# Optimization experiments

Measured on AMD Instinct MI355X. Metric: run time of the kernel, lower is better.

## Reference

```python
import jax, jax.numpy as jnp
import numpy as np

N_NODES = 50000
N_EDGES = 1600000
IN_DIM, HID_DIM, OUT_DIM = 512, 256, 128
N_IDX = 8192


def _graph_conv(x, src, dst, W, b, n_nodes):
    # DGL GraphConv, norm='both': D_dst^{-1/2} A D_src^{-1/2} x W + b
    ones = jnp.ones(src.shape[0], dtype=x.dtype)
    deg_out = jax.ops.segment_sum(ones, src, num_segments=n_nodes)
    deg_in = jax.ops.segment_sum(ones, dst, num_segments=n_nodes)
    ns = jax.lax.rsqrt(jnp.maximum(deg_out, 1.0))  # source norm
    nd = jax.lax.rsqrt(jnp.maximum(deg_in, 1.0))   # dest norm
    msg = (x * ns[:, None])[src]                   # gather [E, F]
    agg = jax.ops.segment_sum(msg, dst, num_segments=n_nodes)
    return (agg * nd[:, None]) @ W + b


def _gcn(x, src, dst, W1, b1, W2, b2, n_nodes):
    h = jax.nn.relu(_graph_conv(x, src, dst, W1, b1, n_nodes))
    return _graph_conv(h, src, dst, W2, b2, n_nodes)


def setup_inputs() -> dict:
    key = jax.random.key(0)
    ks = jax.random.split(key, 16)
    d = {
        'raw1': jax.random.normal(ks[0], (N_NODES, IN_DIM), jnp.float32),
        'raw2': jax.random.normal(ks[1], (N_NODES, IN_DIM), jnp.float32),
        'src1': jax.random.randint(ks[2], (N_EDGES,), 0, N_NODES),
        'dst1': jax.random.randint(ks[3], (N_EDGES,), 0, N_NODES),
        'src2': jax.random.randint(ks[4], (N_EDGES,), 0, N_NODES),
        'dst2': jax.random.randint(ks[5], (N_EDGES,), 0, N_NODES),
        'index': jax.random.randint(ks[6], (N_IDX,), 0, N_NODES),
    }
    def lin(k, fi, fo):
        s = 1.0 / np.sqrt(fi)
        return jax.random.uniform(k, (fi, fo), jnp.float32, -s, s)
    d['e1_W1'] = lin(ks[7], IN_DIM, HID_DIM); d['e1_b1'] = jnp.zeros(HID_DIM, jnp.float32)
    d['e1_W2'] = lin(ks[8], HID_DIM, OUT_DIM); d['e1_b2'] = jnp.zeros(OUT_DIM, jnp.float32)
    d['e2_W1'] = lin(ks[9], IN_DIM, HID_DIM); d['e2_b1'] = jnp.zeros(HID_DIM, jnp.float32)
    d['e2_W2'] = lin(ks[10], HID_DIM, OUT_DIM); d['e2_b2'] = jnp.zeros(OUT_DIM, jnp.float32)
    return d


def reference(raw1, raw2, src1, dst1, src2, dst2, index,
              e1_W1, e1_b1, e1_W2, e1_b2, e2_W1, e2_b1, e2_W2, e2_b2):
    n = raw1.shape[0]
    c1 = _gcn(raw1, src1, dst1, e1_W1, e1_b1, e1_W2, e1_b2, n)[index]
    c2 = _gcn(raw2, src2, dst2, e2_W1, e2_b1, e2_W2, e2_b2, n)[index]
    # F.normalize(dim=1), eps=1e-12
    c1 = c1 / jnp.maximum(jnp.linalg.norm(c1, axis=1, keepdims=True), 1e-12)
    c2 = c2 / jnp.maximum(jnp.linalg.norm(c2, axis=1, keepdims=True), 1e-12)
    z1 = c1 @ c1.T
    z2 = c2 @ c2.T
    z3 = c1 @ c2.T
    z3 = (z3 + z3.T) * 0.5
    z = (z1 + z2 + z3) * (1.0 / 3.0)
    return jnp.triu(z)
```

## Files before the change

kernel.cpp:

```cpp
#include <hip/hip_runtime.h>
#include <hip/hip_bf16.h>

using u16 = unsigned short;
using u32 = unsigned int;

typedef __attribute__((ext_vector_type(8))) short short8;
typedef __attribute__((ext_vector_type(4))) float f32x4;

__device__ __forceinline__ u16 f2bf_u16(float f) {
    __hip_bfloat16 h = __float2bfloat16(f);
    return __builtin_bit_cast(u16, h);
}
__device__ __forceinline__ float bfu(u32 u) { return __uint_as_float(u << 16); }

static constexpr int NN = 50000;
static constexpr int NE = 1600000;
static constexpr int NIDX = 8192;
static constexpr int NRANGE = 8;
static constexpr int RN = NN / NRANGE;
static constexpr int HCH = 16;
static constexpr int NK = NN * NRANGE;
static constexpr int SAB = (NK + 4095) / 4096;
static constexpr int CAPB = 262144;
static constexpr int PEB = 8192;
static constexpr int PGX = (NE + PEB - 1) / PEB;
static constexpr int CVB = 640;
static constexpr int PSTG = 1536;
static constexpr int ZLB = 64 * 63 / 2;
static constexpr int ZHB = ZLB / 2;
static constexpr int ZUB = 64 * 65 / 2;
static constexpr int AGB = NN / 4;
static constexpr int MT = (NN + 127) / 128;
static constexpr int SCX = 256;


__global__ __launch_bounds__(256)
void partition_kernel(const int* __restrict__ s1, const int* __restrict__ d1,
                      const int* __restrict__ s2, const int* __restrict__ d2,
                      int* __restrict__ bcur, u32* __restrict__ ebuf_d, u16* __restrict__ ebuf_s,
                      const float* __restrict__ W1a, const float* __restrict__ W1b,
                      const float* __restrict__ W2a, const float* __restrict__ W2b,
                      u16* __restrict__ W1t, u16* __restrict__ W2t) {
    if (blockIdx.x >= PGX) {
        int o = (blockIdx.x - PGX) + CVB * blockIdx.y;
        int idx = o * 256 + threadIdx.x;
        if (idx < 131072) {
            int k = idx >> 8, n = idx & 255;
            W1t[(size_t)n * 512 + k] = f2bf_u16(W1a[idx]);
        } else if (idx < 262144) {
            int j = idx - 131072;
            int k = j >> 8, n = j & 255;
            W1t[(size_t)131072 + (size_t)n * 512 + k] = f2bf_u16(W1b[j]);
        } else if (idx < 294912) {
            int j = idx - 262144;
            int k = j >> 7, n = j & 127;
            W2t[(size_t)n * 256 + k] = f2bf_u16(W2a[j]);
        } else if (idx < 327680) {
            int j = idx - 294912;
            int k = j >> 7, n = j & 127;
            W2t[(size_t)32768 + (size_t)n * 256 + k] = f2bf_u16(W2b[j]);
        }
        return;
    }
    __shared__ u32 stage_d[8][PSTG];
    __shared__ u16 stage_s[8][PSTG];
    __shared__ int cnt_d[8], cnt_s[8], base_d[8], base_s[8];
    int enc = blockIdx.y;
    const int* s = enc ? s2 : s1;
    const int* d = enc ? d2 : d1;
    if (threadIdx.x < 8) { cnt_d[threadIdx.x] = 0; cnt_s[threadIdx.x] = 0; }
    __syncthreads();
    int* bc_d = bcur + enc * 16;
    int* bc_s = bcur + enc * 16 + 8;
    u32* bd = ebuf_d + (size_t)enc * 8 * CAPB;
    u16* bs = ebuf_s + (size_t)enc * 8 * CAPB;
    int e0 = blockIdx.x * PEB;
    int e1 = min(e0 + PEB, NE);
    for (int e = e0 + threadIdx.x * 4; e < e1; e += 1024) {
        int4 sv = *(const int4*)(s + e);
        int4 dv = *(const int4*)(d + e);
        #pragma unroll
        for (int j = 0; j < 4; ++j) {
            int src = j == 0 ? sv.x : j == 1 ? sv.y : j == 2 ? sv.z : sv.w;
            int dst = j == 0 ? dv.x : j == 1 ? dv.y : j == 2 ? dv.z : dv.w;
            int rd = dst / RN;
            u32 entry = (u32)src | ((u32)(dst - rd * RN) << 16);
            int slot = atomicAdd(&cnt_d[rd], 1);
            if (slot < PSTG) stage_d[rd][slot] = entry;
            else { int gp = atomicAdd(&bc_d[rd], 1); bd[(size_t)rd * CAPB + gp] = entry; }
            int rs = src / RN;
            int slot2 = atomicAdd(&cnt_s[rs], 1);
            if (slot2 < PSTG) stage_s[rs][slot2] = (u16)(src - rs * RN);
            else { int gp = atomicAdd(&bc_s[rs], 1); bs[(size_t)rs * CAPB + gp] = (u16)(src - rs * RN); }
        }
    }
    __syncthreads();
    if (threadIdx.x < 8) {
        int b = threadIdx.x;
        base_d[b] = atomicAdd(&bc_d[b], min(cnt_d[b], PSTG));
        base_s[b] = atomicAdd(&bc_s[b], min(cnt_s[b], PSTG));
    }
    __syncthreads();
    #pragma unroll
    for (int b = 0; b < 8; ++b) {
        int nb = min(cnt_d[b], PSTG);
        for (int i = threadIdx.x; i < nb; i += 256)
            bd[(size_t)b * CAPB + base_d[b] + i] = stage_d[b][i];
        int ns = min(cnt_s[b], PSTG);
        for (int i = threadIdx.x; i < ns; i += 256)
            bs[(size_t)b * CAPB + base_s[b] + i] = stage_s[b][i];
    }
}


__global__ __launch_bounds__(256)
void bhist_kernel(const u32* __restrict__ ebuf_d, const u16* __restrict__ ebuf_s,
                  const int* __restrict__ bcur,
                  u32* __restrict__ partial2, u32* __restrict__ partial_out) {
    __shared__ u32 sh[RN * 2];
    int stripe = blockIdx.x & 7, chunk = blockIdx.x >> 3;
    int enc = blockIdx.y & 1, type = blockIdx.y >> 1;
    if (type == 0) {
        for (int i = threadIdx.x; i < RN * 2; i += 256) sh[i] = 0;
        __syncthreads();
        int size = bcur[enc * 16 + stripe];
        int cs = (size + HCH - 1) / HCH;
        int lo = chunk * cs, hi = min(lo + cs, size);
        const u32* b = ebuf_d + ((size_t)enc * 8 + stripe) * CAPB;
        for (int i = lo + threadIdx.x; i < hi; i += 256) {
            u32 e = b[i];
            u32 idx = (e >> 16) * 8 + (e & 0xffffu) / RN;
            atomicAdd(&sh[idx >> 2], 1u << ((idx & 3) * 8));
        }
        __syncthreads();
        u32* p2 = partial2 + ((size_t)enc * HCH + chunk) * (NN * 2) + stripe * (RN * 2);
        for (int i = threadIdx.x; i < RN * 2; i += 256) p2[i] = sh[i];
    } else {
        for (int i = threadIdx.x; i < RN / 2; i += 256) sh[i] = 0;
        __syncthreads();
        int size = bcur[enc * 16 + 8 + stripe];
        int cs = (size + HCH - 1) / HCH;
        int lo = chunk * cs, hi = min(lo + cs, size);
        const u16* b = ebuf_s + ((size_t)enc * 8 + stripe) * CAPB;
        for (int i = lo + threadIdx.x; i < hi; i += 256) {
            u32 sl = b[i];
            atomicAdd(&sh[sl >> 1], 1u << ((sl & 1) * 16));
        }
        __syncthreads();
        u32* po = partial_out + ((size_t)enc * HCH + chunk) * (NN / 2) + stripe * (RN / 2);
        for (int i = threadIdx.x; i < RN / 2; i += 256) po[i] = sh[i];
    }
}

__global__ void reduce_hist_kernel(const u32* __restrict__ partial2,
                                   const u32* __restrict__ partial_out,
                                   int* __restrict__ deg2, float* __restrict__ norms) {
    int i = blockIdx.x * blockDim.x + threadIdx.x;
    if (i >= 2 * NN) return;
    int enc = i / NN;
    int dst = i - enc * NN;
    int cnt[8];
    #pragma unroll
    for (int r = 0; r < 8; ++r) cnt[r] = 0;
    for (int c = 0; c < HCH; ++c) {
        const u32* p = partial2 + ((size_t)enc * HCH + c) * (NN * 2) + dst * 2;
        u32 w0 = p[0], w1 = p[1];
        cnt[0] += w0 & 0xff; cnt[1] += (w0 >> 8) & 0xff; cnt[2] += (w0 >> 16) & 0xff; cnt[3] += w0 >> 24;
        cnt[4] += w1 & 0xff; cnt[5] += (w1 >> 8) & 0xff; cnt[6] += (w1 >> 16) & 0xff; cnt[7] += w1 >> 24;
    }
    int* dp = deg2 + (size_t)enc * NK + dst * 8;
    int din = 0;
    #pragma unroll
    for (int r = 0; r < 8; ++r) { dp[r] = cnt[r]; din += cnt[r]; }
    norms[(enc * 2 + 1) * NN + dst] = rsqrtf(fmaxf((float)din, 1.f));
    int dout = 0;
    for (int c = 0; c < HCH; ++c) {
        u32 w = partial_out[((size_t)enc * HCH + c) * (NN / 2) + (dst >> 1)];
        dout += (w >> ((dst & 1) * 16)) & 0xffff;
    }
    norms[(enc * 2 + 0) * NN + dst] = rsqrtf(fmaxf((float)dout, 1.f));
}


__global__ __launch_bounds__(1024)
void scanA_kernel(const int* __restrict__ deg2, int* __restrict__ rp2_all, int* __restrict__ tot) {
    int enc = blockIdx.y;
    const int* deg = deg2 + (size_t)enc * NK;
    int* rp = rp2_all + (size_t)enc * (NK + 1);
    __shared__ int wsum[16];
    int t = threadIdx.x, lane = t & 63, wid = t >> 6;
    int i0 = blockIdx.x * 4096 + t * 4;
    int4 v = make_int4(0, 0, 0, 0);
    bool in = (i0 + 3 < NK);
    if (in) v = *(const int4*)(deg + i0);
    int s = v.x + v.y + v.z + v.w;
    int x = s;
    #pragma unroll
    for (int d = 1; d < 64; d <<= 1) {
        int y = __shfl_up(x, d, 64);
        if (lane >= d) x += y;
    }
    if (lane == 63) wsum[wid] = x;
    __syncthreads();
    if (t == 0) {
        int run = 0;
        #pragma unroll
        for (int w = 0; w < 16; ++w) { int q = wsum[w]; wsum[w] = run; run += q; }
        tot[enc * SAB + blockIdx.x] = run;
    }
    __syncthreads();
    if (in) {
        int excl = wsum[wid] + x - s;
        rp[i0] = excl;
        rp[i0 + 1] = excl + v.x;
        rp[i0 + 2] = excl + v.x + v.y;
        rp[i0 + 3] = excl + v.x + v.y + v.z;
    }
}

__global__ __launch_bounds__(256)
void scanC_kernel(int* __restrict__ rp2_all, int* __restrict__ cur2_all, const int* __restrict__ tot) {
    int enc = blockIdx.y;
    int* rp = rp2_all + (size_t)enc * (NK + 1);
    int* cur = cur2_all + (size_t)enc * NK;
    int nA = blockIdx.x >> 2;
    int part = 0;
    for (int i = threadIdx.x; i < nA; i += 256) part += tot[enc * SAB + i];
    #pragma unroll
    for (int d = 1; d < 64; d <<= 1) part += __shfl_xor(part, d, 64);
    __shared__ int red[4];
    __shared__ int soff;
    int lane = threadIdx.x & 63, wv = threadIdx.x >> 6;
    if (lane == 0) red[wv] = part;
    __syncthreads();
    if (threadIdx.x == 0) soff = red[0] + red[1] + red[2] + red[3];
    __syncthreads();
    int off = soff;
    int idx = (blockIdx.x * 256 + threadIdx.x) * 4;
    if (idx < NK) {
        int4 v = *(const int4*)(rp + idx);
        v.x += off; v.y += off; v.z += off; v.w += off;
        *(int4*)(rp + idx) = v;
        *(int4*)(cur + idx) = v;
    }
    if (blockIdx.x == 0 && threadIdx.x == 0) rp[NK] = NE;
}


__device__ __forceinline__ void scatter_body(const u32* __restrict__ ebuf_d,
                                             const int* __restrict__ bcur,
                                             int* __restrict__ cur2_all, u16* __restrict__ csr_all,
                                             int stripe, int chunk, int enc) {
    int size = bcur[enc * 16 + stripe];
    int cs = (size + 63) / 64;
    int lo = chunk * cs, hi = min(lo + cs, size);
    const u32* b = ebuf_d + ((size_t)enc * 8 + stripe) * CAPB;
    int* cursor = cur2_all + (size_t)enc * NK;
    u16* csr = csr_all + (size_t)enc * NE;
    int base = stripe * RN;
    for (int i = lo + threadIdx.x; i < hi; i += 256) {
        u32 e = b[i];
        int src = e & 0xffff;
        int dst = base + (int)(e >> 16);
        int key = dst * 8 + src / RN;
        int pos = atomicAdd(&cursor[key], 1);
        csr[pos] = (u16)src;
    }
}


template<bool A_F32, bool OUT_BF16, bool TRIANG, bool SCALE>
__device__ __forceinline__ void gemm_device(const void* __restrict__ A_, const u16* __restrict__ Bt,
                                            void* __restrict__ C_, const float* __restrict__ rowscale,
                                            int M, int N, int K, int it, int jt, u16* smem) {
    int t = threadIdx.x;
    int brow = it * 128, bcol = jt * 128;
    float* Cf = (float*)C_;
    u16* As = smem;
    u16* Bs = smem + 128 * 40;
    int lane = t & 63, wv = t >> 6;
    int wr = wv >> 1, wc = wv & 1;
    f32x4 acc[4][4];
    #pragma unroll
    for (int m = 0; m < 4; ++m)
        #pragma unroll
        for (int n = 0; n < 4; ++n) acc[m][n] = f32x4{0.f, 0.f, 0.f, 0.f};

    float4 a_f0[4], a_f1[4];
    uint4  a_h0[2], a_h1[2];
    uint4  b_h0[2], b_h1[2];

#define LOADT(S, kk) do {                                                          \
    if constexpr (A_F32) {                                                         \
        const float* A = (const float*)A_;                                         \
        _Pragma("unroll")                                                          \
        for (int p = 0; p < 4; ++p) {                                              \
            int r = p * 32 + (t >> 3), c = (t & 7) * 4;                            \
            int gr = brow + r;                                                     \
            a_f##S[p] = make_float4(0.f, 0.f, 0.f, 0.f);                           \
            if (gr < M) a_f##S[p] = *(const float4*)(A + (size_t)gr * K + (kk) + c); \
        }                                                                          \
    } else {                                                                       \
        const u16* A = (const u16*)A_;                                             \
        _Pragma("unroll")                                                          \
        for (int p = 0; p < 2; ++p) {                                              \
            int r = p * 64 + (t >> 2), c = (t & 3) * 8;                            \
            int gr = brow + r;                                                     \
            a_h##S[p] = make_uint4(0u, 0u, 0u, 0u);                                \
            if (gr < M) a_h##S[p] = *(const uint4*)(A + (size_t)gr * K + (kk) + c); \
        }                                                                          \
    }                                                                              \
    _Pragma("unroll")                                                              \
    for (int p = 0; p < 2; ++p) {                                                  \
        int r = p * 64 + (t >> 2), c = (t & 3) * 8;                                \
        int gn = bcol + r;                                                         \
        b_h##S[p] = make_uint4(0u, 0u, 0u, 0u);                                    \
        if (gn < N) b_h##S[p] = *(const uint4*)(Bt + (size_t)gn * K + (kk) + c);   \
    }                                                                              \
} while (0)

#define STORET(S) do {                                                             \
    if constexpr (A_F32) {                                                         \
        _Pragma("unroll")                                                          \
        for (int p = 0; p < 4; ++p) {                                              \
            int r = p * 32 + (t >> 3), c = (t & 7) * 4;                            \
            u32 lo = (u32)f2bf_u16(a_f##S[p].x) | ((u32)f2bf_u16(a_f##S[p].y) << 16); \
            u32 hi = (u32)f2bf_u16(a_f##S[p].z) | ((u32)f2bf_u16(a_f##S[p].w) << 16); \
            *(uint2*)&As[r * 40 + c] = make_uint2(lo, hi);                         \
        }                                                                          \
    } else {                                                                       \
        _Pragma("unroll")                                                          \
        for (int p = 0; p < 2; ++p) {                                              \
            int r = p * 64 + (t >> 2), c = (t & 3) * 8;                            \
            *(uint4*)&As[r * 40 + c] = a_h##S[p];                                  \
        }                                                                          \
    }                                                                              \
    _Pragma("unroll")                                                              \
    for (int p = 0; p < 2; ++p) {                                                  \
        int r = p * 64 + (t >> 2), c = (t & 3) * 8;                                \
        *(uint4*)&Bs[r * 40 + c] = b_h##S[p];                                      \
    }                                                                              \
} while (0)

    auto compute = [&]() {
        int kg = (lane >> 4) * 8;
        short8 av[4], bv[4];
        #pragma unroll
        for (int m = 0; m < 4; ++m)
            av[m] = *(const short8*)&As[(wr * 64 + m * 16 + (lane & 15)) * 40 + kg];
        #pragma unroll
        for (int n = 0; n < 4; ++n)
            bv[n] = *(const short8*)&Bs[(wc * 64 + n * 16 + (lane & 15)) * 40 + kg];
        #pragma unroll
        for (int m = 0; m < 4; ++m)
            #pragma unroll
            for (int n = 0; n < 4; ++n)
                acc[m][n] = __builtin_amdgcn_mfma_f32_16x16x32_bf16(av[m], bv[n], acc[m][n], 0, 0, 0);
    };

    LOADT(0, 0);
    LOADT(1, 32);
    for (int k0 = 0; k0 < K; k0 += 64) {
        STORET(0);
        __syncthreads();
        if (k0 + 64 < K) LOADT(0, k0 + 64);
        compute();
        __syncthreads();
        STORET(1);
        __syncthreads();
        if (k0 + 96 < K) LOADT(1, k0 + 96);
        compute();
        __syncthreads();
    }
#undef LOADT
#undef STORET

    const int lane15 = lane & 15, lanehi = lane >> 4;
    if (OUT_BF16) {
        u16* stg = smem + wv * 1024;
        #pragma unroll
        for (int m = 0; m < 4; ++m) {
            #pragma unroll
            for (int n = 0; n < 4; ++n)
                #pragma unroll
                for (int r = 0; r < 4; ++r) {
                    float v = acc[m][n][r];
                    if (SCALE) v *= rowscale[brow + wr * 64 + m * 16 + lanehi * 4 + r];
                    stg[(lanehi * 4 + r) * 64 + n * 16 + lane15] = f2bf_u16(v);
                }
            #pragma unroll
            for (int pass = 0; pass < 2; ++pass) {
                int lr = pass * 8 + (lane >> 3);
                int grow = brow + wr * 64 + m * 16 + lr;
                uint4 w = *(uint4*)&stg[lr * 64 + (lane & 7) * 8];
                if (grow < M)
                    *(uint4*)((u16*)C_ + (size_t)grow * N + bcol + wc * 64 + (lane & 7) * 8) = w;
            }
        }
    } else {
        float* stg = (float*)smem + wv * 1024;
        #pragma unroll
        for (int m = 0; m < 4; ++m) {
            #pragma unroll
            for (int n = 0; n < 4; ++n)
                #pragma unroll
                for (int r = 0; r < 4; ++r) {
                    int row = brow + wr * 64 + m * 16 + lanehi * 4 + r;
                    int col = bcol + wc * 64 + n * 16 + lane15;
                    float v = acc[m][n][r];
                    if (SCALE) v *= rowscale[row];
                    if (TRIANG && col < row) v = 0.f;
                    stg[(lanehi * 4 + r) * 64 + n * 16 + lane15] = v;
                }
            #pragma unroll
            for (int pass = 0; pass < 4; ++pass) {
                int lr = pass * 4 + lanehi;
                int grow = brow + wr * 64 + m * 16 + lr;
                f32x4 w = *(f32x4*)&stg[lr * 64 + lane15 * 4];
                if (grow < M) {
                    float* dp = Cf + (size_t)grow * N + bcol + wc * 64 + lane15 * 4;
                    if (TRIANG) __builtin_nontemporal_store(w, (f32x4*)dp);
                    else *(f32x4*)dp = w;
                }
            }
        }
    }
}

__global__ __launch_bounds__(256)
void gemm1scat_kernel(const float* __restrict__ raw0, const float* __restrict__ raw1,
                      const u16* __restrict__ W1t, u16* __restrict__ Y1,
                      const float* __restrict__ norms,
                      const u32* __restrict__ ebuf_d, const int* __restrict__ bcur,
                      int* __restrict__ tick, int* __restrict__ cur2, u16* __restrict__ csr_all) {
    if (blockIdx.x >= MT) {
        u32 lin = blockIdx.x + gridDim.x * (blockIdx.y + gridDim.y * blockIdx.z);
        int stripe = lin & 7;
        __shared__ int tsh;
        if (threadIdx.x == 0) tsh = atomicAdd(&tick[stripe], 1);
        __syncthreads();
        int tkt = tsh;
        scatter_body(ebuf_d, bcur, cur2, csr_all, stripe, tkt & 63, tkt >> 6);
        return;
    }
    __shared__ alignas(16) u16 smem[128 * 40 * 2];
    int enc = blockIdx.z;
    gemm_device<true, true, false, true>(
        enc ? raw1 : raw0, W1t + (size_t)enc * 512 * 256,
        Y1 + (size_t)enc * NN * 256, norms + (size_t)2 * enc * NN,
        NN, 256, 512, blockIdx.x, blockIdx.y, smem);
}

__global__ __launch_bounds__(256)
void gemm2_kernel(const u16* __restrict__ H1, const u16* __restrict__ W2t,
                  u16* __restrict__ Y2, const float* __restrict__ norms) {
    __shared__ alignas(16) u16 smem[128 * 40 * 2];
    int enc = blockIdx.z;
    gemm_device<false, true, false, true>(
        H1 + (size_t)enc * NN * 256, W2t + (size_t)enc * 256 * 128,
        Y2 + (size_t)enc * NN * 128, norms + (size_t)2 * enc * NN,
        NN, 128, 256, blockIdx.x, 0, smem);
}

__global__ __launch_bounds__(256)
void zgemm_kernel(const u16* __restrict__ R, float* __restrict__ out) {
    int b = blockIdx.x;
    int i = (int)((129.0f - sqrtf(129.f * 129.f - 8.f * b)) * 0.5f);
    while ((i + 1) * (129 - (i + 1)) / 2 <= b) ++i;
    while (i * (129 - i) / 2 > b) --i;
    int it = i;
    int jt = i + (b - i * (129 - i) / 2);
    __shared__ alignas(16) u16 smem[128 * 40 * 2];
    gemm_device<false, false, true, false>(R, R, out, nullptr, NIDX, NIDX, 256, it, jt, smem);
}


template<int F, bool RELU, bool OUT_BF16, bool ZFILL>
__global__ __launch_bounds__(256)
void agg_kernel(const u16* __restrict__ Yall, const int* __restrict__ rp2_all,
                const u16* __restrict__ csr_all, const float* __restrict__ norms,
                const float* __restrict__ bias0, const float* __restrict__ bias1,
                void* __restrict__ out_all, float* __restrict__ zout) {
    constexpr int VPL = F / 64;
    int enc = blockIdx.y;
    int bid = blockIdx.x;
    if (ZFILL) {
        if (bid < ZHB) {
            int b = enc * ZHB + bid;
            float fit = (sqrtf(8.f * b + 1.f) + 1.f) * 0.5f;
            int it = (int)fit;
            if (it * (it - 1) / 2 > b) --it;
            else if ((it + 1) * it / 2 <= b) ++it;
            int jt = b - it * (it - 1) / 2;
            int brow = it * 128, bcol = jt * 128;
            f32x4 z = {0.f, 0.f, 0.f, 0.f};
            #pragma unroll
            for (int pq = 0; pq < 16; ++pq) {
                int idx = pq * 256 + threadIdx.x;
                int r = idx >> 5, c4 = idx & 31;
                __builtin_nontemporal_store(z, (f32x4*)(zout + (size_t)(brow + r) * NIDX + bcol + c4 * 4));
            }
            return;
        }
        bid -= ZHB;
    }
    const u16* Y = Yall + (size_t)enc * NN * F;
    const int* rp2 = rp2_all + (size_t)enc * (NK + 1);
    const u16* csr = csr_all + (size_t)enc * NE;
    const float* nd = norms + (size_t)(2 * enc + 1) * NN;
    const float* bias = enc ? bias1 : bias0;
    int lane = threadIdx.x & 63;
    int node = bid * 4 + (threadIdx.x >> 6);
    int e0 = rp2[node * 8], e1 = rp2[node * 8 + 8];
    float acc[VPL];
    #pragma unroll
    for (int j = 0; j < VPL; ++j) acc[j] = 0.f;
    const int off = lane * VPL;

    int e = e0;
    for (; e < e1 && (e & 7) != 0; ++e) {
        int s = csr[e];
        uint2 d = *(const uint2*)(Y + (size_t)s * F + off);
        acc[0] += bfu(d.x & 0xffffu); acc[1] += bfu(d.x >> 16);
        acc[2] += bfu(d.y & 0xffffu); acc[3] += bfu(d.y >> 16);
    }
    for (; e + 16 <= e1; e += 16) {
        uint4 ia = *(const uint4*)(csr + e);
        uint4 ib = *(const uint4*)(csr + e + 8);
        int s0 = ia.x & 0xffff, s1 = ia.x >> 16, s2 = ia.y & 0xffff, s3 = ia.y >> 16;
        int s4 = ia.z & 0xffff, s5 = ia.z >> 16, s6 = ia.w & 0xffff, s7 = ia.w >> 16;
        int s8 = ib.x & 0xffff, s9 = ib.x >> 16, sa = ib.y & 0xffff, sb = ib.y >> 16;
        int sc = ib.z & 0xffff, sd = ib.z >> 16, se = ib.w & 0xffff, sf = ib.w >> 16;
        uint2 d0 = *(const uint2*)(Y + (size_t)s0 * F + off);
        uint2 d1 = *(const uint2*)(Y + (size_t)s1 * F + off);
        uint2 d2 = *(const uint2*)(Y + (size_t)s2 * F + off);
        uint2 d3 = *(const uint2*)(Y + (size_t)s3 * F + off);
        uint2 d4 = *(const uint2*)(Y + (size_t)s4 * F + off);
        uint2 d5 = *(const uint2*)(Y + (size_t)s5 * F + off);
        uint2 d6 = *(const uint2*)(Y + (size_t)s6 * F + off);
        uint2 d7 = *(const uint2*)(Y + (size_t)s7 * F + off);
        uint2 d8 = *(const uint2*)(Y + (size_t)s8 * F + off);
        uint2 d9 = *(const uint2*)(Y + (size_t)s9 * F + off);
        uint2 da = *(const uint2*)(Y + (size_t)sa * F + off);
        uint2 db = *(const uint2*)(Y + (size_t)sb * F + off);
        uint2 dc = *(const uint2*)(Y + (size_t)sc * F + off);
        uint2 dd = *(const uint2*)(Y + (size_t)sd * F + off);
        uint2 de = *(const uint2*)(Y + (size_t)se * F + off);
        uint2 df = *(const uint2*)(Y + (size_t)sf * F + off);
        acc[0] += bfu(d0.x & 0xffffu); acc[1] += bfu(d0.x >> 16); acc[2] += bfu(d0.y & 0xffffu); acc[3] += bfu(d0.y >> 16);
        acc[0] += bfu(d1.x & 0xffffu); acc[1] += bfu(d1.x >> 16); acc[2] += bfu(d1.y & 0xffffu); acc[3] += bfu(d1.y >> 16);
        acc[0] += bfu(d2.x & 0xffffu); acc[1] += bfu(d2.x >> 16); acc[2] += bfu(d2.y & 0xffffu); acc[3] += bfu(d2.y >> 16);
        acc[0] += bfu(d3.x & 0xffffu); acc[1] += bfu(d3.x >> 16); acc[2] += bfu(d3.y & 0xffffu); acc[3] += bfu(d3.y >> 16);
        acc[0] += bfu(d4.x & 0xffffu); acc[1] += bfu(d4.x >> 16); acc[2] += bfu(d4.y & 0xffffu); acc[3] += bfu(d4.y >> 16);
        acc[0] += bfu(d5.x & 0xffffu); acc[1] += bfu(d5.x >> 16); acc[2] += bfu(d5.y & 0xffffu); acc[3] += bfu(d5.y >> 16);
        acc[0] += bfu(d6.x & 0xffffu); acc[1] += bfu(d6.x >> 16); acc[2] += bfu(d6.y & 0xffffu); acc[3] += bfu(d6.y >> 16);
        acc[0] += bfu(d7.x & 0xffffu); acc[1] += bfu(d7.x >> 16); acc[2] += bfu(d7.y & 0xffffu); acc[3] += bfu(d7.y >> 16);
        acc[0] += bfu(d8.x & 0xffffu); acc[1] += bfu(d8.x >> 16); acc[2] += bfu(d8.y & 0xffffu); acc[3] += bfu(d8.y >> 16);
        acc[0] += bfu(d9.x & 0xffffu); acc[1] += bfu(d9.x >> 16); acc[2] += bfu(d9.y & 0xffffu); acc[3] += bfu(d9.y >> 16);
        acc[0] += bfu(da.x & 0xffffu); acc[1] += bfu(da.x >> 16); acc[2] += bfu(da.y & 0xffffu); acc[3] += bfu(da.y >> 16);
        acc[0] += bfu(db.x & 0xffffu); acc[1] += bfu(db.x >> 16); acc[2] += bfu(db.y & 0xffffu); acc[3] += bfu(db.y >> 16);
        acc[0] += bfu(dc.x & 0xffffu); acc[1] += bfu(dc.x >> 16); acc[2] += bfu(dc.y & 0xffffu); acc[3] += bfu(dc.y >> 16);
        acc[0] += bfu(dd.x & 0xffffu); acc[1] += bfu(dd.x >> 16); acc[2] += bfu(dd.y & 0xffffu); acc[3] += bfu(dd.y >> 16);
        acc[0] += bfu(de.x & 0xffffu); acc[1] += bfu(de.x >> 16); acc[2] += bfu(de.y & 0xffffu); acc[3] += bfu(de.y >> 16);
        acc[0] += bfu(df.x & 0xffffu); acc[1] += bfu(df.x >> 16); acc[2] += bfu(df.y & 0xffffu); acc[3] += bfu(df.y >> 16);
    }
    for (; e + 8 <= e1; e += 8) {
        uint4 iv = *(const uint4*)(csr + e);
        int s0 = iv.x & 0xffff, s1 = iv.x >> 16;
        int s2 = iv.y & 0xffff, s3 = iv.y >> 16;
        int s4 = iv.z & 0xffff, s5 = iv.z >> 16;
        int s6 = iv.w & 0xffff, s7 = iv.w >> 16;
        uint2 d0 = *(const uint2*)(Y + (size_t)s0 * F + off);
        uint2 d1 = *(const uint2*)(Y + (size_t)s1 * F + off);
        uint2 d2 = *(const uint2*)(Y + (size_t)s2 * F + off);
        uint2 d3 = *(const uint2*)(Y + (size_t)s3 * F + off);
        uint2 d4 = *(const uint2*)(Y + (size_t)s4 * F + off);
        uint2 d5 = *(const uint2*)(Y + (size_t)s5 * F + off);
        uint2 d6 = *(const uint2*)(Y + (size_t)s6 * F + off);
        uint2 d7 = *(const uint2*)(Y + (size_t)s7 * F + off);
        acc[0] += bfu(d0.x & 0xffffu); acc[1] += bfu(d0.x >> 16); acc[2] += bfu(d0.y & 0xffffu); acc[3] += bfu(d0.y >> 16);
        acc[0] += bfu(d1.x & 0xffffu); acc[1] += bfu(d1.x >> 16); acc[2] += bfu(d1.y & 0xffffu); acc[3] += bfu(d1.y >> 16);
        acc[0] += bfu(d2.x & 0xffffu); acc[1] += bfu(d2.x >> 16); acc[2] += bfu(d2.y & 0xffffu); acc[3] += bfu(d2.y >> 16);
        acc[0] += bfu(d3.x & 0xffffu); acc[1] += bfu(d3.x >> 16); acc[2] += bfu(d3.y & 0xffffu); acc[3] += bfu(d3.y >> 16);
        acc[0] += bfu(d4.x & 0xffffu); acc[1] += bfu(d4.x >> 16); acc[2] += bfu(d4.y & 0xffffu); acc[3] += bfu(d4.y >> 16);
        acc[0] += bfu(d5.x & 0xffffu); acc[1] += bfu(d5.x >> 16); acc[2] += bfu(d5.y & 0xffffu); acc[3] += bfu(d5.y >> 16);
        acc[0] += bfu(d6.x & 0xffffu); acc[1] += bfu(d6.x >> 16); acc[2] += bfu(d6.y & 0xffffu); acc[3] += bfu(d6.y >> 16);
        acc[0] += bfu(d7.x & 0xffffu); acc[1] += bfu(d7.x >> 16); acc[2] += bfu(d7.y & 0xffffu); acc[3] += bfu(d7.y >> 16);
    }
    for (; e < e1; ++e) {
        int s = csr[e];
        uint2 d = *(const uint2*)(Y + (size_t)s * F + off);
        acc[0] += bfu(d.x & 0xffffu); acc[1] += bfu(d.x >> 16);
        acc[2] += bfu(d.y & 0xffffu); acc[3] += bfu(d.y >> 16);
    }

    float ndv = nd[node];
    #pragma unroll
    for (int j = 0; j < VPL; ++j) {
        float o = acc[j] * ndv + bias[off + j];
        if (RELU) o = fmaxf(o, 0.f);
        ((u16*)out_all)[(size_t)enc * NN * F + (size_t)node * F + off + j] = f2bf_u16(o);
    }
}


__global__ __launch_bounds__(256)
void aggr_kernel(const u16* __restrict__ Y2all, const int* __restrict__ rp2_all,
                 const u16* __restrict__ csr_all, const float* __restrict__ norms,
                 const float* __restrict__ b2a, const float* __restrict__ b2b,
                 const int* __restrict__ index, u16* __restrict__ R) {
    int pos = blockIdx.x * 4 + (threadIdx.x >> 6);
    int lane = threadIdx.x & 63;
    int node = index[pos];
    const int off = lane * 2;
    float cx[2], cy[2];
    #pragma unroll
    for (int enc = 0; enc < 2; ++enc) {
        const u16* Y = Y2all + (size_t)enc * NN * 128;
        const int* rp2 = rp2_all + (size_t)enc * (NK + 1);
        const u16* csr = csr_all + (size_t)enc * NE;
        int e0 = rp2[node * 8], e1 = rp2[node * 8 + 8];
        float a0 = 0.f, a1 = 0.f;
        int e = e0;
        for (; e < e1 && (e & 7) != 0; ++e) {
            int s = csr[e];
            u32 d = *(const u32*)(Y + (size_t)s * 128 + off);
            a0 += bfu(d & 0xffffu); a1 += bfu(d >> 16);
        }
        for (; e + 8 <= e1; e += 8) {
            uint4 iv = *(const uint4*)(csr + e);
            int s0 = iv.x & 0xffff, s1 = iv.x >> 16;
            int s2 = iv.y & 0xffff, s3 = iv.y >> 16;
            int s4 = iv.z & 0xffff, s5 = iv.z >> 16;
            int s6 = iv.w & 0xffff, s7 = iv.w >> 16;
            u32 d0 = *(const u32*)(Y + (size_t)s0 * 128 + off);
            u32 d1 = *(const u32*)(Y + (size_t)s1 * 128 + off);
            u32 d2 = *(const u32*)(Y + (size_t)s2 * 128 + off);
            u32 d3 = *(const u32*)(Y + (size_t)s3 * 128 + off);
            u32 d4 = *(const u32*)(Y + (size_t)s4 * 128 + off);
            u32 d5 = *(const u32*)(Y + (size_t)s5 * 128 + off);
            u32 d6 = *(const u32*)(Y + (size_t)s6 * 128 + off);
            u32 d7 = *(const u32*)(Y + (size_t)s7 * 128 + off);
            a0 += bfu(d0 & 0xffffu); a1 += bfu(d0 >> 16);
            a0 += bfu(d1 & 0xffffu); a1 += bfu(d1 >> 16);
            a0 += bfu(d2 & 0xffffu); a1 += bfu(d2 >> 16);
            a0 += bfu(d3 & 0xffffu); a1 += bfu(d3 >> 16);
            a0 += bfu(d4 & 0xffffu); a1 += bfu(d4 >> 16);
            a0 += bfu(d5 & 0xffffu); a1 += bfu(d5 >> 16);
            a0 += bfu(d6 & 0xffffu); a1 += bfu(d6 >> 16);
            a0 += bfu(d7 & 0xffffu); a1 += bfu(d7 >> 16);
        }
        for (; e < e1; ++e) {
            int s = csr[e];
            u32 d = *(const u32*)(Y + (size_t)s * 128 + off);
            a0 += bfu(d & 0xffffu); a1 += bfu(d >> 16);
        }
        float ndv = norms[(2 * enc + 1) * NN + node];
        const float* bias = enc ? b2b : b2a;
        float o0 = a0 * ndv + bias[off];
        float o1 = a1 * ndv + bias[off + 1];
        float ss = o0 * o0 + o1 * o1;
        #pragma unroll
        for (int dshf = 1; dshf < 64; dshf <<= 1) ss += __shfl_xor(ss, dshf, 64);
        float inv = 1.f / fmaxf(sqrtf(ss), 1e-12f);
        cx[enc] = o0 * inv;
        cy[enc] = o1 * inv;
    }
    const float c2 = 0.5f, c3 = 0.28867513459481287f;
    u16* Rp = R + (size_t)pos * 256;
    u32 w0 = (u32)f2bf_u16((cx[0] + cx[1]) * c2) | ((u32)f2bf_u16((cy[0] + cy[1]) * c2) << 16);
    u32 w1 = (u32)f2bf_u16((cx[0] - cx[1]) * c3) | ((u32)f2bf_u16((cy[0] - cy[1]) * c3) << 16);
    *(u32*)(Rp + off) = w0;
    *(u32*)(Rp + 128 + off) = w1;
}


extern "C" void kernel_launch(void* const* d_in, const int* in_sizes, int n_in,
                              void* d_out, int out_size, void* d_ws, size_t ws_size,
                              hipStream_t stream) {
    (void)in_sizes; (void)n_in; (void)out_size; (void)ws_size;
    const float* raw0 = (const float*)d_in[0];
    const float* raw1 = (const float*)d_in[1];
    const int* src1 = (const int*)d_in[2], *dst1 = (const int*)d_in[3];
    const int* src2 = (const int*)d_in[4], *dst2 = (const int*)d_in[5];
    const int* index = (const int*)d_in[6];
    const float* W1a = (const float*)d_in[7];  const float* b1a = (const float*)d_in[8];
    const float* W2a = (const float*)d_in[9];  const float* b2a = (const float*)d_in[10];
    const float* W1b = (const float*)d_in[11]; const float* b1b = (const float*)d_in[12];
    const float* W2b = (const float*)d_in[13]; const float* b2b = (const float*)d_in[14];

    char* wp = (char*)d_ws;
    auto alloc = [&](size_t bytes) -> char* {
        char* r = wp;
        wp += (bytes + 255) & ~(size_t)255;
        return r;
    };
    float* norms   = (float*)alloc((size_t)4 * NN * 4);
    int*   deg2    = (int*)alloc((size_t)2 * NK * 4);
    int*   rp2     = (int*)alloc((size_t)2 * (NK + 1) * 4);
    int*   cur2    = (int*)alloc((size_t)2 * NK * 4);
    int*   tot     = (int*)alloc((size_t)2 * SAB * 4);
    int*   bcur    = (int*)alloc(48 * 4);
    u16*   csr_all = (u16*)alloc((size_t)2 * NE * 2);
    u16*   W1t     = (u16*)alloc((size_t)2 * 512 * 256 * 2);
    u16*   W2t     = (u16*)alloc((size_t)2 * 256 * 128 * 2);
    u16*   Y1      = (u16*)alloc((size_t)2 * NN * 256 * 2);
    u16*   H1      = (u16*)alloc((size_t)2 * NN * 256 * 2);
    u16*   Y2      = (u16*)alloc((size_t)2 * NN * 128 * 2);
    float* H2      = (float*)alloc((size_t)2 * NN * 128 * 4);
    u16*   R       = (u16*)alloc((size_t)NIDX * 256 * 2);
    int*   tick    = bcur + 32;
    u32* partial2    = (u32*)Y1;
    u32* partial_out = (u32*)H1;
    u32* ebuf_d      = (u32*)Y2;
    u16* ebuf_s      = (u16*)H2;

    hipMemsetAsync(bcur, 0, 48 * 4, stream);
    partition_kernel<<<dim3(PGX + CVB, 2), 256, 0, stream>>>(
        src1, dst1, src2, dst2, bcur, ebuf_d, ebuf_s, W1a, W1b, W2a, W2b, W1t, W2t);
    bhist_kernel<<<dim3(8 * HCH, 4), 256, 0, stream>>>(ebuf_d, ebuf_s, bcur, partial2, partial_out);
    reduce_hist_kernel<<<(2 * NN + 255) / 256, 256, 0, stream>>>(partial2, partial_out, deg2, norms);
    scanA_kernel<<<dim3(SAB, 2), 1024, 0, stream>>>(deg2, rp2, tot);
    scanC_kernel<<<dim3((NK / 4 + 255) / 256, 2), 256, 0, stream>>>(rp2, cur2, tot);

    gemm1scat_kernel<<<dim3(MT + SCX, 2, 2), 256, 0, stream>>>(
        raw0, raw1, W1t, Y1, norms, ebuf_d, bcur, tick, cur2, csr_all);
    agg_kernel<256, true, true, true><<<dim3(ZHB + AGB, 2), 256, 0, stream>>>(
        Y1, rp2, csr_all, norms, b1a, b1b, H1, (float*)d_out);
    gemm2_kernel<<<dim3(MT, 1, 2), 256, 0, stream>>>(H1, W2t, Y2, norms);
    aggr_kernel<<<NIDX / 4, 256, 0, stream>>>(Y2, rp2, csr_all, norms, b2a, b2b, index, R);
    zgemm_kernel<<<dim3(ZUB, 1, 1), 256, 0, stream>>>(R, (float*)d_out);
}
```

Baseline: 528.6 us.

## Restructure layer-1 aggregation to process eight nodes per wave range by range

Replaces the templated one-node-per-wave aggregation with a dedicated layer-1 kernel. Each wave now owns eight destination nodes and walks the eight source-node ranges in an outer loop, so the gathers for all eight nodes hit the same slice of Y1 together. The aim is better L2 reuse of the gathered feature rows, and the output is written as packed vector stores. In exchange it drops the 16- and 8-edge unrolled gather loops, leaving a scalar per-edge loop with less memory-level parallelism, and it launches far fewer blocks.

```diff
diff --git a/kernel.cpp b/kernel.cpp
--- a/kernel.cpp
+++ b/kernel.cpp
@@ -29,7 +29,7 @@
 static constexpr int ZLB = 64 * 63 / 2;
 static constexpr int ZHB = ZLB / 2;
 static constexpr int ZUB = 64 * 65 / 2;
-static constexpr int AGB = NN / 4;
+static constexpr int NAGB = (NN + 31) / 32;
 static constexpr int MT = (NN + 127) / 128;
 static constexpr int SCX = 256;
 
@@ -475,132 +475,79 @@
 }
 
 
-template<int F, bool RELU, bool OUT_BF16, bool ZFILL>
-__global__ __launch_bounds__(256)
-void agg_kernel(const u16* __restrict__ Yall, const int* __restrict__ rp2_all,
-                const u16* __restrict__ csr_all, const float* __restrict__ norms,
-                const float* __restrict__ bias0, const float* __restrict__ bias1,
-                void* __restrict__ out_all, float* __restrict__ zout) {
-    constexpr int VPL = F / 64;
+__global__ __launch_bounds__(256)
+void agg1_kernel(const u16* __restrict__ Yall, const int* __restrict__ rp2_all,
+                 const u16* __restrict__ csr_all, const float* __restrict__ norms,
+                 const float* __restrict__ bias0, const float* __restrict__ bias1,
+                 u16* __restrict__ out_all, float* __restrict__ zout) {
     int enc = blockIdx.y;
     int bid = blockIdx.x;
-    if (ZFILL) {
-        if (bid < ZHB) {
-            int b = enc * ZHB + bid;
-            float fit = (sqrtf(8.f * b + 1.f) + 1.f) * 0.5f;
-            int it = (int)fit;
-            if (it * (it - 1) / 2 > b) --it;
-            else if ((it + 1) * it / 2 <= b) ++it;
-            int jt = b - it * (it - 1) / 2;
-            int brow = it * 128, bcol = jt * 128;
-            f32x4 z = {0.f, 0.f, 0.f, 0.f};
-            #pragma unroll
-            for (int pq = 0; pq < 16; ++pq) {
-                int idx = pq * 256 + threadIdx.x;
-                int r = idx >> 5, c4 = idx & 31;
-                __builtin_nontemporal_store(z, (f32x4*)(zout + (size_t)(brow + r) * NIDX + bcol + c4 * 4));
-            }
-            return;
-        }
-        bid -= ZHB;
-    }
-    const u16* Y = Yall + (size_t)enc * NN * F;
+    if (bid < ZHB) {
+        int b = enc * ZHB + bid;
+        float fit = (sqrtf(8.f * b + 1.f) + 1.f) * 0.5f;
+        int it = (int)fit;
+        if (it * (it - 1) / 2 > b) --it;
+        else if ((it + 1) * it / 2 <= b) ++it;
+        int jt = b - it * (it - 1) / 2;
+        int brow = it * 128, bcol = jt * 128;
+        f32x4 z = {0.f, 0.f, 0.f, 0.f};
+        #pragma unroll
+        for (int pq = 0; pq < 16; ++pq) {
+            int idx = pq * 256 + threadIdx.x;
+            int r = idx >> 5, c4 = idx & 31;
+            __builtin_nontemporal_store(z, (f32x4*)(zout + (size_t)(brow + r) * NIDX + bcol + c4 * 4));
+        }
+        return;
+    }
+    bid -= ZHB;
+    const u16* Y = Yall + (size_t)enc * NN * 256;
     const int* rp2 = rp2_all + (size_t)enc * (NK + 1);
     const u16* csr = csr_all + (size_t)enc * NE;
     const float* nd = norms + (size_t)(2 * enc + 1) * NN;
     const float* bias = enc ? bias1 : bias0;
-    int lane = threadIdx.x & 63;
-    int node = bid * 4 + (threadIdx.x >> 6);
-    int e0 = rp2[node * 8], e1 = rp2[node * 8 + 8];
-    float acc[VPL];
-    #pragma unroll
-    for (int j = 0; j < VPL; ++j) acc[j] = 0.f;
-    const int off = lane * VPL;
-
-    int e = e0;
-    for (; e < e1 && (e & 7) != 0; ++e) {
-        int s = csr[e];
-        uint2 d = *(const uint2*)(Y + (size_t)s * F + off);
-        acc[0] += bfu(d.x & 0xffffu); acc[1] += bfu(d.x >> 16);
-        acc[2] += bfu(d.y & 0xffffu); acc[3] += bfu(d.y >> 16);
-    }
-    for (; e + 16 <= e1; e += 16) {
-        uint4 ia = *(const uint4*)(csr + e);
-        uint4 ib = *(const uint4*)(csr + e + 8);
-        int s0 = ia.x & 0xffff, s1 = ia.x >> 16, s2 = ia.y & 0xffff, s3 = ia.y >> 16;
-        int s4 = ia.z & 0xffff, s5 = ia.z >> 16, s6 = ia.w & 0xffff, s7 = ia.w >> 16;
-        int s8 = ib.x & 0xffff, s9 = ib.x >> 16, sa = ib.y & 0xffff, sb = ib.y >> 16;
-        int sc = ib.z & 0xffff, sd = ib.z >> 16, se = ib.w & 0xffff, sf = ib.w >> 16;
-        uint2 d0 = *(const uint2*)(Y + (size_t)s0 * F + off);
-        uint2 d1 = *(const uint2*)(Y + (size_t)s1 * F + off);
-        uint2 d2 = *(const uint2*)(Y + (size_t)s2 * F + off);
-        uint2 d3 = *(const uint2*)(Y + (size_t)s3 * F + off);
-        uint2 d4 = *(const uint2*)(Y + (size_t)s4 * F + off);
-        uint2 d5 = *(const uint2*)(Y + (size_t)s5 * F + off);
-        uint2 d6 = *(const uint2*)(Y + (size_t)s6 * F + off);
-        uint2 d7 = *(const uint2*)(Y + (size_t)s7 * F + off);
-        uint2 d8 = *(const uint2*)(Y + (size_t)s8 * F + off);
-        uint2 d9 = *(const uint2*)(Y + (size_t)s9 * F + off);
-        uint2 da = *(const uint2*)(Y + (size_t)sa * F + off);
-        uint2 db = *(const uint2*)(Y + (size_t)sb * F + off);
-        uint2 dc = *(const uint2*)(Y + (size_t)sc * F + off);
-        uint2 dd = *(const uint2*)(Y + (size_t)sd * F + off);
-        uint2 de = *(const uint2*)(Y + (size_t)se * F + off);
-        uint2 df = *(const uint2*)(Y + (size_t)sf * F + off);
-        acc[0] += bfu(d0.x & 0xffffu); acc[1] += bfu(d0.x >> 16); acc[2] += bfu(d0.y & 0xffffu); acc[3] += bfu(d0.y >> 16);
-        acc[0] += bfu(d1.x & 0xffffu); acc[1] += bfu(d1.x >> 16); acc[2] += bfu(d1.y & 0xffffu); acc[3] += bfu(d1.y >> 16);
-        acc[0] += bfu(d2.x & 0xffffu); acc[1] += bfu(d2.x >> 16); acc[2] += bfu(d2.y & 0xffffu); acc[3] += bfu(d2.y >> 16);
-        acc[0] += bfu(d3.x & 0xffffu); acc[1] += bfu(d3.x >> 16); acc[2] += bfu(d3.y & 0xffffu); acc[3] += bfu(d3.y >> 16);
-        acc[0] += bfu(d4.x & 0xffffu); acc[1] += bfu(d4.x >> 16); acc[2] += bfu(d4.y & 0xffffu); acc[3] += bfu(d4.y >> 16);
-        acc[0] += bfu(d5.x & 0xffffu); acc[1] += bfu(d5.x >> 16); acc[2] += bfu(d5.y & 0xffffu); acc[3] += bfu(d5.y >> 16);
-        acc[0] += bfu(d6.x & 0xffffu); acc[1] += bfu(d6.x >> 16); acc[2] += bfu(d6.y & 0xffffu); acc[3] += bfu(d6.y >> 16);
-        acc[0] += bfu(d7.x & 0xffffu); acc[1] += bfu(d7.x >> 16); acc[2] += bfu(d7.y & 0xffffu); acc[3] += bfu(d7.y >> 16);
-        acc[0] += bfu(d8.x & 0xffffu); acc[1] += bfu(d8.x >> 16); acc[2] += bfu(d8.y & 0xffffu); acc[3] += bfu(d8.y >> 16);
-        acc[0] += bfu(d9.x & 0xffffu); acc[1] += bfu(d9.x >> 16); acc[2] += bfu(d9.y & 0xffffu); acc[3] += bfu(d9.y >> 16);
-        acc[0] += bfu(da.x & 0xffffu); acc[1] += bfu(da.x >> 16); acc[2] += bfu(da.y & 0xffffu); acc[3] += bfu(da.y >> 16);
-        acc[0] += bfu(db.x & 0xffffu); acc[1] += bfu(db.x >> 16); acc[2] += bfu(db.y & 0xffffu); acc[3] += bfu(db.y >> 16);
-        acc[0] += bfu(dc.x & 0xffffu); acc[1] += bfu(dc.x >> 16); acc[2] += bfu(dc.y & 0xffffu); acc[3] += bfu(dc.y >> 16);
-        acc[0] += bfu(dd.x & 0xffffu); acc[1] += bfu(dd.x >> 16); acc[2] += bfu(dd.y & 0xffffu); acc[3] += bfu(dd.y >> 16);
-        acc[0] += bfu(de.x & 0xffffu); acc[1] += bfu(de.x >> 16); acc[2] += bfu(de.y & 0xffffu); acc[3] += bfu(de.y >> 16);
-        acc[0] += bfu(df.x & 0xffffu); acc[1] += bfu(df.x >> 16); acc[2] += bfu(df.y & 0xffffu); acc[3] += bfu(df.y >> 16);
-    }
-    for (; e + 8 <= e1; e += 8) {
-        uint4 iv = *(const uint4*)(csr + e);
-        int s0 = iv.x & 0xffff, s1 = iv.x >> 16;
-        int s2 = iv.y & 0xffff, s3 = iv.y >> 16;
-        int s4 = iv.z & 0xffff, s5 = iv.z >> 16;
-        int s6 = iv.w & 0xffff, s7 = iv.w >> 16;
-        uint2 d0 = *(const uint2*)(Y + (size_t)s0 * F + off);
-        uint2 d1 = *(const uint2*)(Y + (size_t)s1 * F + off);
-        uint2 d2 = *(const uint2*)(Y + (size_t)s2 * F + off);
-        uint2 d3 = *(const uint2*)(Y + (size_t)s3 * F + off);
-        uint2 d4 = *(const uint2*)(Y + (size_t)s4 * F + off);
-        uint2 d5 = *(const uint2*)(Y + (size_t)s5 * F + off);
-        uint2 d6 = *(const uint2*)(Y + (size_t)s6 * F + off);
-        uint2 d7 = *(const uint2*)(Y + (size_t)s7 * F + off);
-        acc[0] += bfu(d0.x & 0xffffu); acc[1] += bfu(d0.x >> 16); acc[2] += bfu(d0.y & 0xffffu); acc[3] += bfu(d0.y >> 16);
-        acc[0] += bfu(d1.x & 0xffffu); acc[1] += bfu(d1.x >> 16); acc[2] += bfu(d1.y & 0xffffu); acc[3] += bfu(d1.y >> 16);
-        acc[0] += bfu(d2.x & 0xffffu); acc[1] += bfu(d2.x >> 16); acc[2] += bfu(d2.y & 0xffffu); acc[3] += bfu(d2.y >> 16);
-        acc[0] += bfu(d3.x & 0xffffu); acc[1] += bfu(d3.x >> 16); acc[2] += bfu(d3.y & 0xffffu); acc[3] += bfu(d3.y >> 16);
-        acc[0] += bfu(d4.x & 0xffffu); acc[1] += bfu(d4.x >> 16); acc[2] += bfu(d4.y & 0xffffu); acc[3] += bfu(d4.y >> 16);
-        acc[0] += bfu(d5.x & 0xffffu); acc[1] += bfu(d5.x >> 16); acc[2] += bfu(d5.y & 0xffffu); acc[3] += bfu(d5.y >> 16);
-        acc[0] += bfu(d6.x & 0xffffu); acc[1] += bfu(d6.x >> 16); acc[2] += bfu(d6.y & 0xffffu); acc[3] += bfu(d6.y >> 16);
-        acc[0] += bfu(d7.x & 0xffffu); acc[1] += bfu(d7.x >> 16); acc[2] += bfu(d7.y & 0xffffu); acc[3] += bfu(d7.y >> 16);
-    }
-    for (; e < e1; ++e) {
-        int s = csr[e];
-        uint2 d = *(const uint2*)(Y + (size_t)s * F + off);
-        acc[0] += bfu(d.x & 0xffffu); acc[1] += bfu(d.x >> 16);
-        acc[2] += bfu(d.y & 0xffffu); acc[3] += bfu(d.y >> 16);
-    }
-
-    float ndv = nd[node];
-    #pragma unroll
-    for (int j = 0; j < VPL; ++j) {
-        float o = acc[j] * ndv + bias[off + j];
-        if (RELU) o = fmaxf(o, 0.f);
-        ((u16*)out_all)[(size_t)enc * NN * F + (size_t)node * F + off + j] = f2bf_u16(o);
-    }
+    int w = threadIdx.x >> 6, lane = threadIdx.x & 63;
+    int nbase = bid * 32 + w * 8;
+    const int off = lane * 4;
+    f32x4 acc0 = {0,0,0,0}, acc1 = {0,0,0,0}, acc2 = {0,0,0,0}, acc3 = {0,0,0,0};
+    f32x4 acc4 = {0,0,0,0}, acc5 = {0,0,0,0}, acc6 = {0,0,0,0}, acc7 = {0,0,0,0};
+
+#define GATH(ACC, NODE_K) do {                                                     \
+    int node = nbase + (NODE_K);                                                   \
+    if (node < NN) {                                                               \
+        int e0 = rp2[node * 8 + r], e1 = rp2[node * 8 + r + 1];                    \
+        for (int e = e0; e < e1; ++e) {                                            \
+            int s = csr[e];                                                        \
+            uint2 dd = *(const uint2*)(Y + (size_t)s * 256 + off);                 \
+            ACC[0] += bfu(dd.x & 0xffffu); ACC[1] += bfu(dd.x >> 16);              \
+            ACC[2] += bfu(dd.y & 0xffffu); ACC[3] += bfu(dd.y >> 16);              \
+        }                                                                          \
+    }                                                                              \
+} while (0)
+
+    for (int r = 0; r < 8; ++r) {
+        GATH(acc0, 0); GATH(acc1, 1); GATH(acc2, 2); GATH(acc3, 3);
+        GATH(acc4, 4); GATH(acc5, 5); GATH(acc6, 6); GATH(acc7, 7);
+    }
+#undef GATH
+
+#define EMIT(ACC, NODE_K) do {                                                     \
+    int node = nbase + (NODE_K);                                                   \
+    if (node < NN) {                                                               \
+        float ndv = nd[node];                                                      \
+        float o0 = fmaxf(ACC[0] * ndv + bias[off], 0.f);                           \
+        float o1 = fmaxf(ACC[1] * ndv + bias[off + 1], 0.f);                       \
+        float o2 = fmaxf(ACC[2] * ndv + bias[off + 2], 0.f);                       \
+        float o3 = fmaxf(ACC[3] * ndv + bias[off + 3], 0.f);                       \
+        uint2 wv2;                                                                 \
+        wv2.x = (u32)f2bf_u16(o0) | ((u32)f2bf_u16(o1) << 16);                     \
+        wv2.y = (u32)f2bf_u16(o2) | ((u32)f2bf_u16(o3) << 16);                     \
+        *(uint2*)(out_all + (size_t)enc * NN * 256 + (size_t)node * 256 + off) = wv2; \
+    }                                                                              \
+} while (0)
+
+    EMIT(acc0, 0); EMIT(acc1, 1); EMIT(acc2, 2); EMIT(acc3, 3);
+    EMIT(acc4, 4); EMIT(acc5, 5); EMIT(acc6, 6); EMIT(acc7, 7);
+#undef EMIT
 }
 
 
@@ -725,7 +672,7 @@
 
     gemm1scat_kernel<<<dim3(MT + SCX, 2, 2), 256, 0, stream>>>(
         raw0, raw1, W1t, Y1, norms, ebuf_d, bcur, tick, cur2, csr_all);
-    agg_kernel<256, true, true, true><<<dim3(ZHB + AGB, 2), 256, 0, stream>>>(
+    agg1_kernel<<<dim3(ZHB + NAGB, 2), 256, 0, stream>>>(
         Y1, rp2, csr_all, norms, b1a, b1b, H1, (float*)d_out);
     gemm2_kernel<<<dim3(MT, 1, 2), 256, 0, stream>>>(H1, W2t, Y2, norms);
     aggr_kernel<<<NIDX / 4, 256, 0, stream>>>(Y2, rp2, csr_all, norms, b2a, b2b, index, R);
```

After: 703.2 us. +33.0%, slower.
